# Optimization experiments

Hardware: AMD Instinct MI355X
Metric: run time of the kernel (lower is better)

The kernel has to match this reference:

```python
import jax, jax.numpy as jnp
import numpy as np

EMBED_DIM = 1024
NUM_HEADS = 16
BLOCK_SIZE = 128
GLOBAL_EVERY = 24


def make_block_sparse_mask(seq_len):
    # 0 where allowed, -inf where disallowed. Allowed iff same block, or
    # either position lies in a 'global' block (block index % global_every == 0).
    bi = jnp.arange(seq_len) // BLOCK_SIZE
    is_global = (bi % GLOBAL_EVERY) == 0
    allowed = (bi[:, None] == bi[None, :]) | is_global[:, None] | is_global[None, :]
    return jnp.where(allowed, 0.0, -jnp.inf).astype(jnp.float32)


def setup_inputs() -> dict:
    key = jax.random.key(0)
    k_x, k_w, k_wo = jax.random.split(key, 3)
    B, L, D = 1, 4096, EMBED_DIM
    x = jax.random.normal(k_x, (B, L, D), dtype=jnp.float32)
    # nn.MultiheadAttention params: packed in_proj [3D, D] + bias [3D], out_proj [D, D] + bias [D]
    w_qkv = jax.random.normal(k_w, (3 * D, D), dtype=jnp.float32) * 0.02
    b_qkv = jnp.zeros((3 * D,), dtype=jnp.float32)
    w_out = jax.random.normal(k_wo, (D, D), dtype=jnp.float32) * 0.02
    b_out = jnp.zeros((D,), dtype=jnp.float32)
    return {"x": x, "w_qkv": w_qkv, "b_qkv": b_qkv, "w_out": w_out, "b_out": b_out}


def reference(x, w_qkv, b_qkv, w_out, b_out):
    B, L, D = x.shape
    H = NUM_HEADS
    hd = D // H
    mask = make_block_sparse_mask(L)  # [L, L] additive
    qkv = x @ w_qkv.T + b_qkv  # [B, L, 3D]
    q, k, v = jnp.split(qkv, 3, axis=-1)
    # [B, H, L, hd]
    q = q.reshape(B, L, H, hd).transpose(0, 2, 1, 3)
    k = k.reshape(B, L, H, hd).transpose(0, 2, 1, 3)
    v = v.reshape(B, L, H, hd).transpose(0, 2, 1, 3)
    scale = 1.0 / jnp.sqrt(jnp.asarray(hd, dtype=x.dtype))
    scores = jnp.einsum('bhqd,bhkd->bhqk', q * scale, k) + mask  # [B, H, L, L]
    attn = jax.nn.softmax(scores, axis=-1)
    out = jnp.einsum('bhqk,bhkd->bhqd', attn, v)  # [B, H, L, hd]
    out = out.transpose(0, 2, 1, 3).reshape(B, L, D)
    return out @ w_out.T + b_out
```

## Files before the change

### kernel.cpp

```cpp
#include <hip/hip_runtime.h>
#include <hip/hip_bf16.h>
#include <math.h>


#define SEQ 4096
#define DIM 1024
#define NHEADS 16
#define HDIM 64
#define BS 128
#define ESTRIDE 136

using short8 = __attribute__((ext_vector_type(8))) short;
using floatx4 = __attribute__((ext_vector_type(4))) float;

__device__ __forceinline__ float bf2f(short s) {
  unsigned u = ((unsigned)(unsigned short)s) << 16;
  return __uint_as_float(u);
}

__device__ __forceinline__ unsigned pack_bf16(float a, float b) {
  __hip_bfloat16 ba = __float2bfloat16(a);
  __hip_bfloat16 bb = __float2bfloat16(b);
  return ((unsigned)*(unsigned short*)&bb << 16) | (unsigned)*(unsigned short*)&ba;
}

__device__ __forceinline__ void gld_lds16(const __hip_bfloat16* g, __hip_bfloat16* l) {
  __builtin_amdgcn_global_load_lds(
      (const __attribute__((address_space(1))) unsigned int*)g,
      (__attribute__((address_space(3))) unsigned int*)l, 16, 0, 0);
}

__global__ __launch_bounds__(256) void downcast3(
    const float* __restrict__ x, const float* __restrict__ wq,
    const float* __restrict__ wo, __hip_bfloat16* __restrict__ xd,
    __hip_bfloat16* __restrict__ wqd, __hip_bfloat16* __restrict__ wod) {
  int id = blockIdx.x;
  const float* src;
  __hip_bfloat16* dst;
  int base;
  if (id < 4096) { src = x; dst = xd; base = id; }
  else if (id < 7168) { src = wq; dst = wqd; base = id - 4096; }
  else { src = wo; dst = wod; base = id - 7168; }
  int i = (base * 256 + threadIdx.x) * 4;
  float4 v = *(const float4*)(src + i);
  __hip_bfloat16 b0 = __float2bfloat16(v.x);
  __hip_bfloat16 b1 = __float2bfloat16(v.y);
  __hip_bfloat16 b2 = __float2bfloat16(v.z);
  __hip_bfloat16 b3 = __float2bfloat16(v.w);
  ushort4 packed = {*(unsigned short*)&b0, *(unsigned short*)&b1,
                    *(unsigned short*)&b2, *(unsigned short*)&b3};
  *(ushort4*)(((unsigned short*)dst) + i) = packed;
}

__global__ __launch_bounds__(256) void gemm_qkv(const __hip_bfloat16* __restrict__ Amat,
                                                const __hip_bfloat16* __restrict__ Wmat,
                                                const float* __restrict__ Bias,
                                                __hip_bfloat16* __restrict__ qkv) {
  __shared__ __align__(16) char pool[128 * ESTRIDE * 2];
  __hip_bfloat16* Asmem = (__hip_bfloat16*)pool;
  __hip_bfloat16* Bsmem = (__hip_bfloat16*)(pool + 8192);
  __hip_bfloat16* Ep = (__hip_bfloat16*)pool;

  const int Kd = DIM;
  const int t = threadIdx.x;
  const int w = t >> 6;
  const int lane = t & 63;
  const int fr = lane & 15;
  const int quad = lane >> 4;
  const int wm = w >> 1, wn = w & 1;

  int id = blockIdx.x;
  int xcd = id & 7, j = id >> 3;
  int m_idx = xcd + (j & 3) * 8;
  int n_idx = j >> 2;
  const int m0 = m_idx * 128;
  const int n0 = n_idx * 128;
  const int s = n0 >> 10;
  const int cc0 = n0 & 1023;
  const bool vmode = (s == 2);

  const __hip_bfloat16* APtr = vmode ? Amat + (size_t)m0 * Kd : Wmat + (size_t)n0 * Kd;
  const __hip_bfloat16* BPtr = vmode ? Wmat + (size_t)n0 * Kd : Amat + (size_t)m0 * Kd;

  floatx4 acc[4][4];
#pragma unroll
  for (int i = 0; i < 4; ++i)
#pragma unroll
    for (int jj = 0; jj < 4; ++jj) acc[i][jj] = (floatx4){0.f, 0.f, 0.f, 0.f};

  for (int kk = 0; kk < Kd / 32; ++kk) {
#pragma unroll
    for (int jj = 0; jj < 2; ++jj) {
      int c = jj * 256 + t;
      int ldso = (jj * 256 + w * 64) * 8;
      gld_lds16(APtr + (size_t)(c >> 2) * Kd + kk * 32 + (c & 3) * 8, &Asmem[ldso]);
      gld_lds16(BPtr + (size_t)(c >> 2) * Kd + kk * 32 + (c & 3) * 8, &Bsmem[ldso]);
    }
    __syncthreads();
    short8 af[4], bf_[4];
#pragma unroll
    for (int mt = 0; mt < 4; ++mt)
      af[mt] = *(const short8*)&Asmem[(wm * 64 + mt * 16 + fr) * 32 + quad * 8];
#pragma unroll
    for (int nt = 0; nt < 4; ++nt)
      bf_[nt] = *(const short8*)&Bsmem[(wn * 64 + nt * 16 + fr) * 32 + quad * 8];
#pragma unroll
    for (int mt = 0; mt < 4; ++mt)
#pragma unroll
      for (int nt = 0; nt < 4; ++nt)
        acc[mt][nt] = __builtin_amdgcn_mfma_f32_16x16x32_bf16(af[mt], bf_[nt],
                                                              acc[mt][nt], 0, 0, 0);
    __syncthreads();
  }

#pragma unroll
  for (int nt = 0; nt < 4; ++nt) {
    int dcol = wn * 64 + nt * 16 + fr;
#pragma unroll
    for (int mt = 0; mt < 4; ++mt) {
      int drow0 = wm * 64 + mt * 16 + quad * 4;
      ushort4 pk;
      unsigned short* pks = (unsigned short*)&pk;
#pragma unroll
      for (int i = 0; i < 4; ++i) {
        __hip_bfloat16 bb = __float2bfloat16(acc[mt][nt][i]);
        pks[i] = *(unsigned short*)&bb;
      }
      *(ushort4*)&Ep[dcol * ESTRIDE + drow0] = pk;
    }
  }
  __syncthreads();

  if (!vmode) {
    __hip_bfloat16* dst = qkv + (size_t)s * SEQ * DIM;
#pragma unroll
    for (int rr = 0; rr < 8; ++rr) {
      int m = rr * 16 + (t >> 4);
      int ch = (t & 15) * 8;
      short8 v8 = *(const short8*)&Ep[m * ESTRIDE + ch];
      float4 b0 = *(const float4*)&Bias[n0 + ch];
      float4 b1 = *(const float4*)&Bias[n0 + ch + 4];
      float bb[8] = {b0.x, b0.y, b0.z, b0.w, b1.x, b1.y, b1.z, b1.w};
      short8 o8;
#pragma unroll
      for (int k = 0; k < 8; ++k) {
        __hip_bfloat16 ob = __float2bfloat16(bf2f(v8[k]) + bb[k]);
        o8[k] = *(short*)&ob;
      }
      *(short8*)&dst[(size_t)(m0 + m) * DIM + cc0 + ch] = o8;
    }
  } else {
    __hip_bfloat16* vt = qkv + 2ull * SEQ * DIM;
#pragma unroll
    for (int rr = 0; rr < 8; ++rr) {
      int nrow = rr * 16 + (t >> 4);
      int ch = (t & 15) * 8;
      float bv = Bias[n0 + nrow];
      short8 v8 = *(const short8*)&Ep[nrow * ESTRIDE + ch];
      short8 o8;
#pragma unroll
      for (int k = 0; k < 8; ++k) {
        __hip_bfloat16 ob = __float2bfloat16(bf2f(v8[k]) + bv);
        o8[k] = *(short*)&ob;
      }
      *(short8*)&vt[(size_t)(cc0 + nrow) * SEQ + m0 + ch] = o8;
    }
  }
}

__global__ __launch_bounds__(256) void gemm_out(const __hip_bfloat16* __restrict__ Amat,
                                                const __hip_bfloat16* __restrict__ Wmat,
                                                const float* __restrict__ Bias,
                                                float* __restrict__ out) {
  __shared__ __align__(16) __hip_bfloat16 Asmem[128 * 32];
  __shared__ __align__(16) __hip_bfloat16 Bsmem[64 * 32];
  const int Kd = DIM;
  const int t = threadIdx.x;
  const int w = t >> 6;
  const int lane = t & 63;
  const int fr = lane & 15;
  const int quad = lane >> 4;
  const int wm = w >> 1, wn = w & 1;
  int id = blockIdx.x;
  int xcd = id & 7, j = id >> 3;
  int m_idx = xcd + (j & 3) * 8;
  int n_idx = j >> 2;
  const int m0 = m_idx * 128;
  const int n0 = n_idx * 64;
  const __hip_bfloat16* Ablk = Amat + (size_t)m0 * Kd;
  const __hip_bfloat16* Bblk = Wmat + (size_t)n0 * Kd;
  floatx4 acc[4][2];
#pragma unroll
  for (int i = 0; i < 4; ++i)
#pragma unroll
    for (int jj = 0; jj < 2; ++jj) acc[i][jj] = (floatx4){0.f, 0.f, 0.f, 0.f};
  for (int kk = 0; kk < Kd / 32; ++kk) {
#pragma unroll
    for (int jj = 0; jj < 2; ++jj) {
      int c = jj * 256 + t;
      int ldso = (jj * 256 + w * 64) * 8;
      gld_lds16(Ablk + (size_t)(c >> 2) * Kd + kk * 32 + (c & 3) * 8, &Asmem[ldso]);
    }
    gld_lds16(Bblk + (size_t)(t >> 2) * Kd + kk * 32 + (t & 3) * 8, &Bsmem[t * 8]);
    __syncthreads();
    short8 af[4], bf_[2];
#pragma unroll
    for (int mt = 0; mt < 4; ++mt)
      af[mt] = *(const short8*)&Asmem[(wm * 64 + mt * 16 + fr) * 32 + quad * 8];
#pragma unroll
    for (int nt = 0; nt < 2; ++nt)
      bf_[nt] = *(const short8*)&Bsmem[(wn * 32 + nt * 16 + fr) * 32 + quad * 8];
#pragma unroll
    for (int mt = 0; mt < 4; ++mt)
#pragma unroll
      for (int nt = 0; nt < 2; ++nt)
        acc[mt][nt] = __builtin_amdgcn_mfma_f32_16x16x32_bf16(af[mt], bf_[nt],
                                                              acc[mt][nt], 0, 0, 0);
    __syncthreads();
  }
#pragma unroll
  for (int nt = 0; nt < 2; ++nt) {
    int n = n0 + wn * 32 + nt * 16 + fr;
    float bv = Bias[n];
#pragma unroll
    for (int mt = 0; mt < 4; ++mt) {
      int m = m0 + wm * 64 + mt * 16 + quad * 4;
#pragma unroll
      for (int i = 0; i < 4; ++i)
        out[(size_t)(m + i) * DIM + n] = acc[mt][nt][i] + bv;
    }
  }
}

__global__ __launch_bounds__(256) void attn_mfma(
    const __hip_bfloat16* __restrict__ qkv,
    __hip_bfloat16* __restrict__ aout,
    float* __restrict__ po, float* __restrict__ pm, float* __restrict__ pl) {
  __shared__ __align__(16) __hip_bfloat16 Kbuf[16 * 512];
  __shared__ __align__(16) __hip_bfloat16 Vbuf[16 * 512];
  const int h = blockIdx.y;
  const int wgid = blockIdx.x;
  const int t = threadIdx.x;
  const int wv = t >> 6;
  const int lane = t & 63;
  const int fr = lane & 15;
  const int quad = lane >> 4;

  int qb, q0, niter, slice = 0, pid = 0;
  bool direct;
  if (wgid < 60) {
    int nb = wgid >> 1;
    qb = (nb < 23) ? nb + 1 : nb + 2;
    q0 = qb * BS + (wgid & 1) * 64;
    niter = 3;
    direct = true;
  } else {
    int gi = wgid - 60;
    slice = gi & 7;
    int chunk = gi >> 3;
    qb = (chunk >> 1) * 24;
    q0 = qb * BS + (chunk & 1) * 64;
    niter = 4;
    direct = false;
    pid = (h * 4 + chunk) * 8 + slice;
  }

  const __hip_bfloat16* Q = qkv;
  const __hip_bfloat16* K = qkv + (size_t)SEQ * DIM;
  const __hip_bfloat16* Vt = qkv + 2ull * SEQ * DIM;

  short8 qa0, qa1;
  {
    const __hip_bfloat16* qp =
        Q + (size_t)(q0 + wv * 16 + fr) * DIM + h * HDIM + quad * 8;
    qa0 = *(const short8*)(qp);
    qa1 = *(const short8*)(qp + 32);
  }

  float mrow = -INFINITY, lsum = 0.f;
  floatx4 o[4];
#pragma unroll
  for (int i = 0; i < 4; ++i) o[i] = (floatx4){0.f, 0.f, 0.f, 0.f};

  for (int bi = 0; bi < niter; ++bi) {
    int kb = direct ? (bi == 0 ? 0 : (bi == 1 ? qb : 24)) : slice * 4 + bi;

    const __hip_bfloat16* Kg = K + (size_t)(kb * BS) * DIM + h * HDIM;
    const __hip_bfloat16* Vg = Vt + (size_t)(h * HDIM) * SEQ + kb * BS;
    __syncthreads();
#pragma unroll
    for (int rr = 0; rr < 4; ++rr) {
      int f = rr * 4 + wv;
      int nt = f >> 1, ks = f & 1;
      gld_lds16(Kg + (size_t)(nt * 16 + fr) * DIM + ks * 32 + quad * 8,
                &Kbuf[f * 512]);
      int nt2 = f >> 2, ks2 = f & 3;
      gld_lds16(Vg + (size_t)(nt2 * 16 + fr) * SEQ + ks2 * 32 + quad * 8,
                &Vbuf[f * 512]);
    }
    __syncthreads();

    floatx4 s[8];
#pragma unroll
    for (int nt = 0; nt < 8; ++nt) {
      short8 kf0 = *(const short8*)&Kbuf[(nt * 2 + 0) * 512 + lane * 8];
      short8 kf1 = *(const short8*)&Kbuf[(nt * 2 + 1) * 512 + lane * 8];
      floatx4 acc = {0.f, 0.f, 0.f, 0.f};
      acc = __builtin_amdgcn_mfma_f32_16x16x32_bf16(kf0, qa0, acc, 0, 0, 0);
      acc = __builtin_amdgcn_mfma_f32_16x16x32_bf16(kf1, qa1, acc, 0, 0, 0);
      s[nt] = acc;
    }
#pragma unroll
    for (int nt = 0; nt < 8; ++nt)
#pragma unroll
      for (int i = 0; i < 4; ++i) s[nt][i] *= 0.125f;

    float rmax = -INFINITY;
#pragma unroll
    for (int nt = 0; nt < 8; ++nt)
#pragma unroll
      for (int i = 0; i < 4; ++i) rmax = fmaxf(rmax, s[nt][i]);
    rmax = fmaxf(rmax, __shfl_xor(rmax, 16, 64));
    rmax = fmaxf(rmax, __shfl_xor(rmax, 32, 64));
    float newm = fmaxf(mrow, rmax);
    float alpha = __expf(mrow - newm);
    float psum = 0.f;
    unsigned pki[8][2];
#pragma unroll
    for (int nt = 0; nt < 8; ++nt) {
      float p0 = __expf(s[nt][0] - newm);
      float p1 = __expf(s[nt][1] - newm);
      float p2 = __expf(s[nt][2] - newm);
      float p3 = __expf(s[nt][3] - newm);
      psum += (p0 + p1) + (p2 + p3);
      pki[nt][0] = pack_bf16(p0, p1);
      pki[nt][1] = pack_bf16(p2, p3);
    }
    psum += __shfl_xor(psum, 16, 64);
    psum += __shfl_xor(psum, 32, 64);
    lsum = lsum * alpha + psum;
    mrow = newm;
#pragma unroll
    for (int nt2 = 0; nt2 < 4; ++nt2)
#pragma unroll
      for (int i = 0; i < 4; ++i) o[nt2][i] *= alpha;

    union { int w4[4]; short8 s8; } pw[4];
#pragma unroll
    for (int ks2 = 0; ks2 < 4; ++ks2) {
#pragma unroll
      for (int p = 0; p < 4; ++p) {
        int srcl = fr + ((((quad & 1) << 1) + (p >> 1)) << 4);
        int lo = __shfl((int)pki[2 * ks2][p & 1], srcl, 64);
        int hi = __shfl((int)pki[2 * ks2 + 1][p & 1], srcl, 64);
        pw[ks2].w4[p] = (quad & 2) ? hi : lo;
      }
    }

#pragma unroll
    for (int nt2 = 0; nt2 < 4; ++nt2) {
#pragma unroll
      for (int ks2 = 0; ks2 < 4; ++ks2) {
        short8 vb = *(const short8*)&Vbuf[(nt2 * 4 + ks2) * 512 + lane * 8];
        o[nt2] = __builtin_amdgcn_mfma_f32_16x16x32_bf16(vb, pw[ks2].s8, o[nt2], 0, 0, 0);
      }
    }
  }

  if (direct) {
    float inv = 1.f / lsum;
    __hip_bfloat16* orow = aout + (size_t)(q0 + wv * 16 + fr) * DIM + h * HDIM + quad * 4;
#pragma unroll
    for (int nt2 = 0; nt2 < 4; ++nt2) {
      ushort4 pk;
      unsigned short* pks = (unsigned short*)&pk;
#pragma unroll
      for (int i = 0; i < 4; ++i) {
        __hip_bfloat16 ob = __float2bfloat16(o[nt2][i] * inv);
        pks[i] = *(unsigned short*)&ob;
      }
      *(ushort4*)(orow + nt2 * 16) = pk;
    }
  } else {
    float* pob = po + (size_t)pid * 4096 + (wv * 16 + fr) * 64 + quad * 4;
#pragma unroll
    for (int nt2 = 0; nt2 < 4; ++nt2) {
      float4 v = {o[nt2][0], o[nt2][1], o[nt2][2], o[nt2][3]};
      *(float4*)(pob + nt2 * 16) = v;
    }
    if (quad == 0) {
      pm[pid * 64 + wv * 16 + fr] = mrow;
      pl[pid * 64 + wv * 16 + fr] = lsum;
    }
  }
}

__global__ __launch_bounds__(256) void combine(const float* __restrict__ po,
                                               const float* __restrict__ pm,
                                               const float* __restrict__ pl,
                                               __hip_bfloat16* __restrict__ aout) {
  int b = blockIdx.x;
  int h = b >> 2, chunk = b & 3;
  int t = threadIdx.x;
  int row = t >> 2;
  int d0 = (t & 3) * 16;

  float m8[8];
  float newm = -INFINITY;
#pragma unroll
  for (int s = 0; s < 8; ++s) {
    m8[s] = pm[(b * 8 + s) * 64 + row];
    newm = fmaxf(newm, m8[s]);
  }
  float wgt[8], lsum = 0.f;
#pragma unroll
  for (int s = 0; s < 8; ++s) {
    wgt[s] = __expf(m8[s] - newm);
    lsum += pl[(b * 8 + s) * 64 + row] * wgt[s];
  }
  float acc[16];
#pragma unroll
  for (int jj = 0; jj < 16; ++jj) acc[jj] = 0.f;
#pragma unroll
  for (int s = 0; s < 8; ++s) {
    const float* src = po + ((size_t)(b * 8 + s) * 4096) + row * 64 + d0;
#pragma unroll
    for (int j4 = 0; j4 < 4; ++j4) {
      float4 v = *(const float4*)(src + j4 * 4);
      acc[j4 * 4 + 0] += wgt[s] * v.x;
      acc[j4 * 4 + 1] += wgt[s] * v.y;
      acc[j4 * 4 + 2] += wgt[s] * v.z;
      acc[j4 * 4 + 3] += wgt[s] * v.w;
    }
  }
  float inv = 1.f / lsum;
  int qrow = (chunk >> 1) * 3072 + (chunk & 1) * 64 + row;
#pragma unroll
  for (int jj = 0; jj < 16; ++jj)
    aout[(size_t)qrow * DIM + h * HDIM + d0 + jj] = __float2bfloat16(acc[jj] * inv);
}

extern "C" void kernel_launch(void* const* d_in, const int* in_sizes, int n_in,
                              void* d_out, int out_size, void* d_ws, size_t ws_size,
                              hipStream_t stream) {
  const float* x = (const float*)d_in[0];
  const float* w_qkv = (const float*)d_in[1];
  const float* b_qkv = (const float*)d_in[2];
  const float* w_out = (const float*)d_in[3];
  const float* b_out = (const float*)d_in[4];
  float* out = (float*)d_out;

  char* wsb = (char*)d_ws;
  __hip_bfloat16* qkv_ws = (__hip_bfloat16*)(wsb);
  __hip_bfloat16* x_bf = (__hip_bfloat16*)(wsb + 24ull * 1024 * 1024);
  __hip_bfloat16* wqkv_bf = (__hip_bfloat16*)(wsb + 32ull * 1024 * 1024);
  __hip_bfloat16* wout_bf = (__hip_bfloat16*)(wsb + 38ull * 1024 * 1024);
  __hip_bfloat16* attn_ws = (__hip_bfloat16*)(wsb + 40ull * 1024 * 1024);
  float* po = (float*)(wsb + 24ull * 1024 * 1024);
  float* pm = (float*)(wsb + 32ull * 1024 * 1024);
  float* pl = (float*)(wsb + 32ull * 1024 * 1024 + 131072);

  dim3 blk(256);
  downcast3<<<dim3(8192), blk, 0, stream>>>(x, w_qkv, w_out, x_bf, wqkv_bf, wout_bf);
  gemm_qkv<<<dim3(768), blk, 0, stream>>>(x_bf, wqkv_bf, b_qkv, qkv_ws);
  attn_mfma<<<dim3(92, NHEADS), blk, 0, stream>>>(qkv_ws, attn_ws, po, pm, pl);
  combine<<<dim3(64), blk, 0, stream>>>(po, pm, pl, attn_ws);
  gemm_out<<<dim3(512), blk, 0, stream>>>(attn_ws, wout_bf, b_out, out);
}
```

Baseline: 175.1 us.

## Rewrite QKV GEMM as 256x256 tile, 8-wave, double-buffered pipelined kernel

Replaces the 128x128 single-buffered QKV GEMM with a 256x256 tile per 512-thread block. It uses a 64-deep K step, double-buffered LDS with XOR swizzling, and global-to-LDS loads staged between MFMA phases with split barriers and s_setprio. The epilogue is also rewritten with a swizzled LDS staging layout. The goal is more data reuse per block, loads overlapped with MFMA work, and fewer LDS bank conflicts. The cost is 128KB of LDS per block, only 192 blocks on the GPU, and heavier register pressure.

Result: slower. 182.0 us (+3.9%).

```diff
diff --git a/kernel.cpp b/kernel.cpp
--- a/kernel.cpp
+++ b/kernel.cpp
@@ -8,7 +8,6 @@
 #define NHEADS 16
 #define HDIM 64
 #define BS 128
-#define ESTRIDE 136
 
 using short8 = __attribute__((ext_vector_type(8))) short;
 using floatx4 = __attribute__((ext_vector_type(4))) float;
@@ -52,120 +51,206 @@
   *(ushort4*)(((unsigned short*)dst) + i) = packed;
 }
 
-__global__ __launch_bounds__(256) void gemm_qkv(const __hip_bfloat16* __restrict__ Amat,
-                                                const __hip_bfloat16* __restrict__ Wmat,
-                                                const float* __restrict__ Bias,
-                                                __hip_bfloat16* __restrict__ qkv) {
-  __shared__ __align__(16) char pool[128 * ESTRIDE * 2];
-  __hip_bfloat16* Asmem = (__hip_bfloat16*)pool;
-  __hip_bfloat16* Bsmem = (__hip_bfloat16*)(pool + 8192);
-  __hip_bfloat16* Ep = (__hip_bfloat16*)pool;
-
-  const int Kd = DIM;
+#define NT 16
+
+__global__ __launch_bounds__(512, 2) void gemm_qkv(const __hip_bfloat16* __restrict__ Amat,
+                                                   const __hip_bfloat16* __restrict__ Wmat,
+                                                   const float* __restrict__ Bias,
+                                                   __hip_bfloat16* __restrict__ qkv) {
+  __shared__ __align__(16) char pool[131072];
   const int t = threadIdx.x;
   const int w = t >> 6;
   const int lane = t & 63;
   const int fr = lane & 15;
   const int quad = lane >> 4;
-  const int wm = w >> 1, wn = w & 1;
+  const int wA = w >> 2;
+  const int wB = w & 3;
+  const int bro = (wB & 1) * 64;
 
   int id = blockIdx.x;
-  int xcd = id & 7, j = id >> 3;
-  int m_idx = xcd + (j & 3) * 8;
-  int n_idx = j >> 2;
-  const int m0 = m_idx * 128;
-  const int n0 = n_idx * 128;
+  int swz = (id & 7) * 24 + (id >> 3);
+  int m_idx = swz & 15;
+  int n_idx = swz >> 4;
+  const int m0 = m_idx * 256;
+  const int n0 = n_idx * 256;
   const int s = n0 >> 10;
   const int cc0 = n0 & 1023;
   const bool vmode = (s == 2);
 
-  const __hip_bfloat16* APtr = vmode ? Amat + (size_t)m0 * Kd : Wmat + (size_t)n0 * Kd;
-  const __hip_bfloat16* BPtr = vmode ? Wmat + (size_t)n0 * Kd : Amat + (size_t)m0 * Kd;
-
-  floatx4 acc[4][4];
-#pragma unroll
-  for (int i = 0; i < 4; ++i)
-#pragma unroll
-    for (int jj = 0; jj < 4; ++jj) acc[i][jj] = (floatx4){0.f, 0.f, 0.f, 0.f};
-
-  for (int kk = 0; kk < Kd / 32; ++kk) {
-#pragma unroll
-    for (int jj = 0; jj < 2; ++jj) {
-      int c = jj * 256 + t;
-      int ldso = (jj * 256 + w * 64) * 8;
-      gld_lds16(APtr + (size_t)(c >> 2) * Kd + kk * 32 + (c & 3) * 8, &Asmem[ldso]);
-      gld_lds16(BPtr + (size_t)(c >> 2) * Kd + kk * 32 + (c & 3) * 8, &Bsmem[ldso]);
-    }
-    __syncthreads();
-    short8 af[4], bf_[4];
-#pragma unroll
-    for (int mt = 0; mt < 4; ++mt)
-      af[mt] = *(const short8*)&Asmem[(wm * 64 + mt * 16 + fr) * 32 + quad * 8];
-#pragma unroll
-    for (int nt = 0; nt < 4; ++nt)
-      bf_[nt] = *(const short8*)&Bsmem[(wn * 64 + nt * 16 + fr) * 32 + quad * 8];
-#pragma unroll
-    for (int mt = 0; mt < 4; ++mt)
-#pragma unroll
-      for (int nt = 0; nt < 4; ++nt)
-        acc[mt][nt] = __builtin_amdgcn_mfma_f32_16x16x32_bf16(af[mt], bf_[nt],
-                                                              acc[mt][nt], 0, 0, 0);
-    __syncthreads();
-  }
-
-#pragma unroll
-  for (int nt = 0; nt < 4; ++nt) {
-    int dcol = wn * 64 + nt * 16 + fr;
-#pragma unroll
-    for (int mt = 0; mt < 4; ++mt) {
-      int drow0 = wm * 64 + mt * 16 + quad * 4;
+  const __hip_bfloat16* APtr = vmode ? Amat + (size_t)m0 * DIM : Wmat + (size_t)n0 * DIM;
+  const __hip_bfloat16* BPtr = vmode ? Wmat + (size_t)n0 * DIM : Amat + (size_t)m0 * DIM;
+
+
+  auto STG = [&](int kt, int ab, int h) {
+    const __hip_bfloat16* rowbase = (ab ? BPtr : APtr) + (size_t)(h * 128) * DIM;
+    char* lb = pool + ab * 65536 + (kt & 1) * 32768 + h * 16384;
+#pragma unroll
+    for (int c = 0; c < 2; ++c) {
+      int r = c * 64 + (t >> 3);
+      int g = t & 7;
+      gld_lds16(rowbase + (size_t)r * DIM + kt * 64 + ((g ^ (r & 7)) << 3),
+                (__hip_bfloat16*)(lb + (c * 512 + w * 64) * 16));
+    }
+  };
+
+  auto frag = [&](const char* base, int row, int kk) -> short8 {
+    return *(const short8*)(base + row * 128 +
+                            ((kk * 64 + quad * 16) ^ ((row & 7) << 4)));
+  };
+
+#define SBAR()                            \
+  do {                                    \
+    asm volatile("" ::: "memory");        \
+    __builtin_amdgcn_s_barrier();         \
+    asm volatile("" ::: "memory");        \
+  } while (0)
+
+  STG(0, 0, 0); STG(0, 0, 1); STG(0, 1, 0); STG(0, 1, 1);
+  STG(1, 0, 0); STG(1, 0, 1); STG(1, 1, 0);
+  asm volatile("s_waitcnt vmcnt(6)" ::: "memory");
+  __builtin_amdgcn_s_barrier();
+  asm volatile("" ::: "memory");
+
+  floatx4 acc[8][4];
+#pragma unroll
+  for (int i = 0; i < 8; ++i)
+#pragma unroll
+    for (int j = 0; j < 4; ++j) acc[i][j] = (floatx4){0.f, 0.f, 0.f, 0.f};
+
+  for (int kt = 0; kt < NT; ++kt) {
+    const int d = kt & 1;
+    const char* Al = pool + d * 32768 + wA * 16384;
+    const char* Bl = pool + 65536 + d * 32768 + (wB >> 1) * 16384;
+    short8 af[4][2], bf0[2][2], bf1[2][2];
+
+#pragma unroll
+    for (int at = 0; at < 4; ++at) {
+      af[at][0] = frag(Al, at * 16 + fr, 0);
+      af[at][1] = frag(Al, at * 16 + fr, 1);
+    }
+#pragma unroll
+    for (int bt = 0; bt < 2; ++bt) {
+      bf0[bt][0] = frag(Bl, bro + bt * 16 + fr, 0);
+      bf0[bt][1] = frag(Bl, bro + bt * 16 + fr, 1);
+    }
+    if (kt < NT - 1) STG(kt + 1, 1, 1);
+    __builtin_amdgcn_s_setprio(1);
+#pragma unroll
+    for (int at = 0; at < 4; ++at)
+#pragma unroll
+      for (int bt = 0; bt < 2; ++bt) {
+        acc[at][bt] = __builtin_amdgcn_mfma_f32_16x16x32_bf16(af[at][0], bf0[bt][0], acc[at][bt], 0, 0, 0);
+        acc[at][bt] = __builtin_amdgcn_mfma_f32_16x16x32_bf16(af[at][1], bf0[bt][1], acc[at][bt], 0, 0, 0);
+      }
+    __builtin_amdgcn_s_setprio(0);
+    SBAR();
+
+#pragma unroll
+    for (int bt = 0; bt < 2; ++bt) {
+      bf1[bt][0] = frag(Bl, bro + (bt + 2) * 16 + fr, 0);
+      bf1[bt][1] = frag(Bl, bro + (bt + 2) * 16 + fr, 1);
+    }
+    __builtin_amdgcn_s_setprio(1);
+#pragma unroll
+    for (int at = 0; at < 4; ++at)
+#pragma unroll
+      for (int bt = 0; bt < 2; ++bt) {
+        acc[at][bt + 2] = __builtin_amdgcn_mfma_f32_16x16x32_bf16(af[at][0], bf1[bt][0], acc[at][bt + 2], 0, 0, 0);
+        acc[at][bt + 2] = __builtin_amdgcn_mfma_f32_16x16x32_bf16(af[at][1], bf1[bt][1], acc[at][bt + 2], 0, 0, 0);
+      }
+    __builtin_amdgcn_s_setprio(0);
+    SBAR();
+
+#pragma unroll
+    for (int at = 0; at < 4; ++at) {
+      af[at][0] = frag(Al, (at + 4) * 16 + fr, 0);
+      af[at][1] = frag(Al, (at + 4) * 16 + fr, 1);
+    }
+    if (kt < NT - 2) STG(kt + 2, 1, 0);
+    __builtin_amdgcn_s_setprio(1);
+#pragma unroll
+    for (int at = 0; at < 4; ++at)
+#pragma unroll
+      for (int bt = 0; bt < 2; ++bt) {
+        acc[at + 4][bt + 2] = __builtin_amdgcn_mfma_f32_16x16x32_bf16(af[at][0], bf1[bt][0], acc[at + 4][bt + 2], 0, 0, 0);
+        acc[at + 4][bt + 2] = __builtin_amdgcn_mfma_f32_16x16x32_bf16(af[at][1], bf1[bt][1], acc[at + 4][bt + 2], 0, 0, 0);
+      }
+    __builtin_amdgcn_s_setprio(0);
+    SBAR();
+
+    if (kt < NT - 2) { STG(kt + 2, 0, 0); STG(kt + 2, 0, 1); }
+    __builtin_amdgcn_s_setprio(1);
+#pragma unroll
+    for (int at = 0; at < 4; ++at)
+#pragma unroll
+      for (int bt = 0; bt < 2; ++bt) {
+        acc[at + 4][bt] = __builtin_amdgcn_mfma_f32_16x16x32_bf16(af[at][0], bf0[bt][0], acc[at + 4][bt], 0, 0, 0);
+        acc[at + 4][bt] = __builtin_amdgcn_mfma_f32_16x16x32_bf16(af[at][1], bf0[bt][1], acc[at + 4][bt], 0, 0, 0);
+      }
+    __builtin_amdgcn_s_setprio(0);
+
+    if (kt < NT - 2) asm volatile("s_waitcnt vmcnt(6)" ::: "memory");
+    else             asm volatile("s_waitcnt vmcnt(0)" ::: "memory");
+    __builtin_amdgcn_s_barrier();
+    asm volatile("" ::: "memory");
+  }
+
+#pragma unroll
+  for (int at = 0; at < 8; ++at)
+#pragma unroll
+    for (int bt = 0; bt < 4; ++bt) {
+      int F = wB * 64 + bt * 16 + fr;
+      int q0b = (wA * 128 + at * 16 + quad * 4) * 2;
       ushort4 pk;
       unsigned short* pks = (unsigned short*)&pk;
 #pragma unroll
       for (int i = 0; i < 4; ++i) {
-        __hip_bfloat16 bb = __float2bfloat16(acc[mt][nt][i]);
+        __hip_bfloat16 bb = __float2bfloat16(acc[at][bt][i]);
         pks[i] = *(unsigned short*)&bb;
       }
-      *(ushort4*)&Ep[dcol * ESTRIDE + drow0] = pk;
-    }
-  }
+      *(ushort4*)(pool + F * 512 + (q0b ^ ((F & 7) << 4))) = pk;
+    }
   __syncthreads();
 
-  if (!vmode) {
-    __hip_bfloat16* dst = qkv + (size_t)s * SEQ * DIM;
-#pragma unroll
-    for (int rr = 0; rr < 8; ++rr) {
-      int m = rr * 16 + (t >> 4);
-      int ch = (t & 15) * 8;
-      short8 v8 = *(const short8*)&Ep[m * ESTRIDE + ch];
-      float4 b0 = *(const float4*)&Bias[n0 + ch];
-      float4 b1 = *(const float4*)&Bias[n0 + ch + 4];
-      float bb[8] = {b0.x, b0.y, b0.z, b0.w, b1.x, b1.y, b1.z, b1.w};
-      short8 o8;
-#pragma unroll
-      for (int k = 0; k < 8; ++k) {
-        __hip_bfloat16 ob = __float2bfloat16(bf2f(v8[k]) + bb[k]);
-        o8[k] = *(short*)&ob;
-      }
-      *(short8*)&dst[(size_t)(m0 + m) * DIM + cc0 + ch] = o8;
-    }
-  } else {
-    __hip_bfloat16* vt = qkv + 2ull * SEQ * DIM;
-#pragma unroll
-    for (int rr = 0; rr < 8; ++rr) {
-      int nrow = rr * 16 + (t >> 4);
-      int ch = (t & 15) * 8;
-      float bv = Bias[n0 + nrow];
-      short8 v8 = *(const short8*)&Ep[nrow * ESTRIDE + ch];
-      short8 o8;
-#pragma unroll
-      for (int k = 0; k < 8; ++k) {
-        __hip_bfloat16 ob = __float2bfloat16(bf2f(v8[k]) + bv);
-        o8[k] = *(short*)&ob;
-      }
-      *(short8*)&vt[(size_t)(cc0 + nrow) * SEQ + m0 + ch] = o8;
-    }
-  }
+  {
+    int F = t >> 1;
+    int hh = t & 1;
+    if (!vmode) {
+      __hip_bfloat16* drow = qkv + (size_t)s * SEQ * DIM + (size_t)(m0 + F) * DIM + cc0;
+#pragma unroll
+      for (int g16 = 0; g16 < 16; ++g16) {
+        int G = hh * 16 + g16;
+        short8 v8 = *(const short8*)(pool + F * 512 + ((G << 4) ^ ((F & 7) << 4)));
+        float4 b0 = *(const float4*)&Bias[n0 + G * 8];
+        float4 b1 = *(const float4*)&Bias[n0 + G * 8 + 4];
+        float bbv[8] = {b0.x, b0.y, b0.z, b0.w, b1.x, b1.y, b1.z, b1.w};
+        short8 o8;
+#pragma unroll
+        for (int k = 0; k < 8; ++k) {
+          __hip_bfloat16 ob = __float2bfloat16(bf2f(v8[k]) + bbv[k]);
+          o8[k] = *(short*)&ob;
+        }
+        *(short8*)&drow[G * 8] = o8;
+      }
+    } else {
+      __hip_bfloat16* vt = qkv + 2ull * SEQ * DIM;
+      __hip_bfloat16* drow = vt + (size_t)(cc0 + F) * SEQ + m0;
+      float bv = Bias[n0 + F];
+#pragma unroll
+      for (int g16 = 0; g16 < 16; ++g16) {
+        int G = hh * 16 + g16;
+        short8 v8 = *(const short8*)(pool + F * 512 + ((G << 4) ^ ((F & 7) << 4)));
+        short8 o8;
+#pragma unroll
+        for (int k = 0; k < 8; ++k) {
+          __hip_bfloat16 ob = __float2bfloat16(bf2f(v8[k]) + bv);
+          o8[k] = *(short*)&ob;
+        }
+        *(short8*)&drow[G * 8] = o8;
+      }
+    }
+  }
+#undef SBAR
 }
 
 __global__ __launch_bounds__(256) void gemm_out(const __hip_bfloat16* __restrict__ Amat,
@@ -462,7 +547,7 @@
 
   dim3 blk(256);
   downcast3<<<dim3(8192), blk, 0, stream>>>(x, w_qkv, w_out, x_bf, wqkv_bf, wout_bf);
-  gemm_qkv<<<dim3(768), blk, 0, stream>>>(x_bf, wqkv_bf, b_qkv, qkv_ws);
+  gemm_qkv<<<dim3(192), dim3(512), 0, stream>>>(x_bf, wqkv_bf, b_qkv, qkv_ws);
   attn_mfma<<<dim3(92, NHEADS), blk, 0, stream>>>(qkv_ws, attn_ws, po, pm, pl);
   combine<<<dim3(64), blk, 0, stream>>>(po, pm, pl, attn_ws);
   gemm_out<<<dim3(512), blk, 0, stream>>>(attn_ws, wout_bf, b_out, out);
```

## Fuse split-KV combine into attention via last-block atomic counter

Applied to the files above, without the earlier changes.

Removes the separate combine kernel launch. Each global-block attention workgroup now writes its partial results, issues a threadfence, and atomically increments a per-(head,chunk) counter. The last of the 8 slices then performs the log-sum-exp merge in place. The counters are zeroed inside the downcast kernel, which saves one launch and its tail latency but adds fences and an atomic to the split workgroups.

Result: slower. 289.9 us (+65.5%).

```diff
diff --git a/kernel.cpp b/kernel.cpp
--- a/kernel.cpp
+++ b/kernel.cpp
@@ -33,8 +33,10 @@
 __global__ __launch_bounds__(256) void downcast3(
     const float* __restrict__ x, const float* __restrict__ wq,
     const float* __restrict__ wo, __hip_bfloat16* __restrict__ xd,
-    __hip_bfloat16* __restrict__ wqd, __hip_bfloat16* __restrict__ wod) {
+    __hip_bfloat16* __restrict__ wqd, __hip_bfloat16* __restrict__ wod,
+    int* __restrict__ cnt) {
   int id = blockIdx.x;
+  if (id == 0 && threadIdx.x < 64) cnt[threadIdx.x] = 0;
   const float* src;
   __hip_bfloat16* dst;
   int base;
@@ -235,9 +237,11 @@
 __global__ __launch_bounds__(256) void attn_mfma(
     const __hip_bfloat16* __restrict__ qkv,
     __hip_bfloat16* __restrict__ aout,
-    float* __restrict__ po, float* __restrict__ pm, float* __restrict__ pl) {
+    float* __restrict__ po, float* __restrict__ pm, float* __restrict__ pl,
+    int* __restrict__ cnt) {
   __shared__ __align__(16) __hip_bfloat16 Kbuf[16 * 512];
   __shared__ __align__(16) __hip_bfloat16 Vbuf[16 * 512];
+  __shared__ int lastflag;
   const int h = blockIdx.y;
   const int wgid = blockIdx.x;
   const int t = threadIdx.x;
@@ -246,7 +250,7 @@
   const int fr = lane & 15;
   const int quad = lane >> 4;
 
-  int qb, q0, niter, slice = 0, pid = 0;
+  int qb, q0, niter, slice = 0, pid = 0, chunk = 0;
   bool direct;
   if (wgid < 60) {
     int nb = wgid >> 1;
@@ -257,7 +261,7 @@
   } else {
     int gi = wgid - 60;
     slice = gi & 7;
-    int chunk = gi >> 3;
+    chunk = gi >> 3;
     qb = (chunk >> 1) * 24;
     q0 = qb * BS + (chunk & 1) * 64;
     niter = 4;
@@ -392,52 +396,54 @@
       pm[pid * 64 + wv * 16 + fr] = mrow;
       pl[pid * 64 + wv * 16 + fr] = lsum;
     }
-  }
-}
-
-__global__ __launch_bounds__(256) void combine(const float* __restrict__ po,
-                                               const float* __restrict__ pm,
-                                               const float* __restrict__ pl,
-                                               __hip_bfloat16* __restrict__ aout) {
-  int b = blockIdx.x;
-  int h = b >> 2, chunk = b & 3;
-  int t = threadIdx.x;
-  int row = t >> 2;
-  int d0 = (t & 3) * 16;
-
-  float m8[8];
-  float newm = -INFINITY;
-#pragma unroll
-  for (int s = 0; s < 8; ++s) {
-    m8[s] = pm[(b * 8 + s) * 64 + row];
-    newm = fmaxf(newm, m8[s]);
-  }
-  float wgt[8], lsum = 0.f;
-#pragma unroll
-  for (int s = 0; s < 8; ++s) {
-    wgt[s] = __expf(m8[s] - newm);
-    lsum += pl[(b * 8 + s) * 64 + row] * wgt[s];
-  }
-  float acc[16];
-#pragma unroll
-  for (int jj = 0; jj < 16; ++jj) acc[jj] = 0.f;
-#pragma unroll
-  for (int s = 0; s < 8; ++s) {
-    const float* src = po + ((size_t)(b * 8 + s) * 4096) + row * 64 + d0;
-#pragma unroll
-    for (int j4 = 0; j4 < 4; ++j4) {
-      float4 v = *(const float4*)(src + j4 * 4);
-      acc[j4 * 4 + 0] += wgt[s] * v.x;
-      acc[j4 * 4 + 1] += wgt[s] * v.y;
-      acc[j4 * 4 + 2] += wgt[s] * v.z;
-      acc[j4 * 4 + 3] += wgt[s] * v.w;
-    }
-  }
-  float inv = 1.f / lsum;
-  int qrow = (chunk >> 1) * 3072 + (chunk & 1) * 64 + row;
-#pragma unroll
-  for (int jj = 0; jj < 16; ++jj)
-    aout[(size_t)qrow * DIM + h * HDIM + d0 + jj] = __float2bfloat16(acc[jj] * inv);
+
+    __threadfence();
+    __syncthreads();
+    if (t == 0) {
+      int old = atomicAdd(&cnt[h * 4 + chunk], 1);
+      lastflag = (old == 7);
+    }
+    __syncthreads();
+    if (lastflag) {
+      __threadfence();
+      const int b = h * 4 + chunk;
+      const int row = t >> 2;
+      const int d0 = (t & 3) * 16;
+      float m8[8];
+      float newm = -INFINITY;
+#pragma unroll
+      for (int ss = 0; ss < 8; ++ss) {
+        m8[ss] = pm[(b * 8 + ss) * 64 + row];
+        newm = fmaxf(newm, m8[ss]);
+      }
+      float wgt[8], ls = 0.f;
+#pragma unroll
+      for (int ss = 0; ss < 8; ++ss) {
+        wgt[ss] = __expf(m8[ss] - newm);
+        ls += pl[(b * 8 + ss) * 64 + row] * wgt[ss];
+      }
+      float acc[16];
+#pragma unroll
+      for (int jj = 0; jj < 16; ++jj) acc[jj] = 0.f;
+#pragma unroll
+      for (int ss = 0; ss < 8; ++ss) {
+        const float* src = po + ((size_t)(b * 8 + ss) * 4096) + row * 64 + d0;
+#pragma unroll
+        for (int j4 = 0; j4 < 4; ++j4) {
+          float4 v = *(const float4*)(src + j4 * 4);
+          acc[j4 * 4 + 0] += wgt[ss] * v.x;
+          acc[j4 * 4 + 1] += wgt[ss] * v.y;
+          acc[j4 * 4 + 2] += wgt[ss] * v.z;
+          acc[j4 * 4 + 3] += wgt[ss] * v.w;
+        }
+      }
+      float inv = 1.f / ls;
+      int qrow = (chunk >> 1) * 3072 + (chunk & 1) * 64 + row;
+#pragma unroll
+      for (int jj = 0; jj < 16; ++jj)
+        aout[(size_t)qrow * DIM + h * HDIM + d0 + jj] = __float2bfloat16(acc[jj] * inv);
+    }
+  }
 }
 
 extern "C" void kernel_launch(void* const* d_in, const int* in_sizes, int n_in,
@@ -459,11 +465,11 @@
   float* po = (float*)(wsb + 24ull * 1024 * 1024);
   float* pm = (float*)(wsb + 32ull * 1024 * 1024);
   float* pl = (float*)(wsb + 32ull * 1024 * 1024 + 131072);
+  int* cnt = (int*)(wsb + 48ull * 1024 * 1024);
 
   dim3 blk(256);
-  downcast3<<<dim3(8192), blk, 0, stream>>>(x, w_qkv, w_out, x_bf, wqkv_bf, wout_bf);
+  downcast3<<<dim3(8192), blk, 0, stream>>>(x, w_qkv, w_out, x_bf, wqkv_bf, wout_bf, cnt);
   gemm_qkv<<<dim3(768), blk, 0, stream>>>(x_bf, wqkv_bf, b_qkv, qkv_ws);
-  attn_mfma<<<dim3(92, NHEADS), blk, 0, stream>>>(qkv_ws, attn_ws, po, pm, pl);
-  combine<<<dim3(64), blk, 0, stream>>>(po, pm, pl, attn_ws);
+  attn_mfma<<<dim3(92, NHEADS), blk, 0, stream>>>(qkv_ws, attn_ws, po, pm, pl, cnt);
   gemm_out<<<dim3(512), blk, 0, stream>>>(attn_ws, wout_bf, b_out, out);
 }
```

## Double-buffer K/V tiles in attention kernel to overlap loads with MFMA

Applied to the files above, without the earlier changes.

Attention K/V staging in LDS becomes double-buffered. The next key block's global-to-LDS loads are issued before computing on the current block, using explicit vmcnt waits and raw barriers in place of __syncthreads. The goal is to hide global load latency behind the QK and PV MFMAs. It doubles LDS use to 64KB per workgroup, which may lower occupancy, and each block only runs 3-4 iterations, so there is little to overlap.

Result: slower. 180.8 us (+3.3%).

```diff
diff --git a/kernel.cpp b/kernel.cpp
--- a/kernel.cpp
+++ b/kernel.cpp
@@ -236,8 +236,8 @@
     const __hip_bfloat16* __restrict__ qkv,
     __hip_bfloat16* __restrict__ aout,
     float* __restrict__ po, float* __restrict__ pm, float* __restrict__ pl) {
-  __shared__ __align__(16) __hip_bfloat16 Kbuf[16 * 512];
-  __shared__ __align__(16) __hip_bfloat16 Vbuf[16 * 512];
+  __shared__ __align__(16) __hip_bfloat16 Kbuf[2 * 16 * 512];
+  __shared__ __align__(16) __hip_bfloat16 Vbuf[2 * 16 * 512];
   const int h = blockIdx.y;
   const int wgid = blockIdx.x;
   const int t = threadIdx.x;
@@ -277,34 +277,48 @@
     qa1 = *(const short8*)(qp + 32);
   }
 
-  float mrow = -INFINITY, lsum = 0.f;
-  floatx4 o[4];
-#pragma unroll
-  for (int i = 0; i < 4; ++i) o[i] = (floatx4){0.f, 0.f, 0.f, 0.f};
-
-  for (int bi = 0; bi < niter; ++bi) {
-    int kb = direct ? (bi == 0 ? 0 : (bi == 1 ? qb : 24)) : slice * 4 + bi;
-
+  auto kbof = [&](int bi) -> int {
+    return direct ? (bi == 0 ? 0 : (bi == 1 ? qb : 24)) : slice * 4 + bi;
+  };
+  auto stage = [&](int kb, int d) {
     const __hip_bfloat16* Kg = K + (size_t)(kb * BS) * DIM + h * HDIM;
     const __hip_bfloat16* Vg = Vt + (size_t)(h * HDIM) * SEQ + kb * BS;
-    __syncthreads();
 #pragma unroll
     for (int rr = 0; rr < 4; ++rr) {
       int f = rr * 4 + wv;
       int nt = f >> 1, ks = f & 1;
       gld_lds16(Kg + (size_t)(nt * 16 + fr) * DIM + ks * 32 + quad * 8,
-                &Kbuf[f * 512]);
+                &Kbuf[d * 8192 + f * 512]);
       int nt2 = f >> 2, ks2 = f & 3;
       gld_lds16(Vg + (size_t)(nt2 * 16 + fr) * SEQ + ks2 * 32 + quad * 8,
-                &Vbuf[f * 512]);
-    }
-    __syncthreads();
+                &Vbuf[d * 8192 + f * 512]);
+    }
+  };
+
+  float mrow = -INFINITY, lsum = 0.f;
+  floatx4 o[4];
+#pragma unroll
+  for (int i = 0; i < 4; ++i) o[i] = (floatx4){0.f, 0.f, 0.f, 0.f};
+
+  stage(kbof(0), 0);
+
+  for (int bi = 0; bi < niter; ++bi) {
+    if (bi + 1 < niter) {
+      stage(kbof(bi + 1), (bi + 1) & 1);
+      asm volatile("s_waitcnt vmcnt(8)" ::: "memory");
+    } else {
+      asm volatile("s_waitcnt vmcnt(0)" ::: "memory");
+    }
+    __builtin_amdgcn_s_barrier();
+    asm volatile("" ::: "memory");
+    const __hip_bfloat16* Kb = &Kbuf[(bi & 1) * 8192];
+    const __hip_bfloat16* Vb = &Vbuf[(bi & 1) * 8192];
 
     floatx4 s[8];
 #pragma unroll
     for (int nt = 0; nt < 8; ++nt) {
-      short8 kf0 = *(const short8*)&Kbuf[(nt * 2 + 0) * 512 + lane * 8];
-      short8 kf1 = *(const short8*)&Kbuf[(nt * 2 + 1) * 512 + lane * 8];
+      short8 kf0 = *(const short8*)&Kb[(nt * 2 + 0) * 512 + lane * 8];
+      short8 kf1 = *(const short8*)&Kb[(nt * 2 + 1) * 512 + lane * 8];
       floatx4 acc = {0.f, 0.f, 0.f, 0.f};
       acc = __builtin_amdgcn_mfma_f32_16x16x32_bf16(kf0, qa0, acc, 0, 0, 0);
       acc = __builtin_amdgcn_mfma_f32_16x16x32_bf16(kf1, qa1, acc, 0, 0, 0);
@@ -361,10 +375,13 @@
     for (int nt2 = 0; nt2 < 4; ++nt2) {
 #pragma unroll
       for (int ks2 = 0; ks2 < 4; ++ks2) {
-        short8 vb = *(const short8*)&Vbuf[(nt2 * 4 + ks2) * 512 + lane * 8];
+        short8 vb = *(const short8*)&Vb[(nt2 * 4 + ks2) * 512 + lane * 8];
         o[nt2] = __builtin_amdgcn_mfma_f32_16x16x32_bf16(vb, pw[ks2].s8, o[nt2], 0, 0, 0);
       }
     }
+
+    asm volatile("" ::: "memory");
+    __builtin_amdgcn_s_barrier();
   }
 
   if (direct) {
```
